# Performance work log

Measured on AMD Instinct MI355X. Metric: run time of the kernel, lower is better.

Reference implementation:

```python
import jax, jax.numpy as jnp
import numpy as np

N = 100000      # nodes
E = 1600000     # edges
B = 64          # graphs in batch
V = 10000       # input_dim (embedding vocab)
EMB = 256       # emb_dim
HID = 64        # hidden_dim
OUT = 32        # output_dim


def setup_inputs() -> dict:
    key = jax.random.key(0)
    ks = jax.random.split(key, 12)
    state = jax.random.randint(ks[0], (B, 2), 0, V, dtype=jnp.int32)
    x = jax.random.randint(ks[1], (N,), 0, V, dtype=jnp.int32)
    edge_index = jax.random.randint(ks[2], (2, E), 0, N, dtype=jnp.int32)
    edge_weight = jnp.ones((E,), jnp.float32)
    # contiguous graph assignment (every graph non-empty)
    batch = jnp.minimum(jnp.arange(N, dtype=jnp.int32) // (N // B), B - 1)

    def lin(k, fin, fout):
        return jax.random.normal(k, (fin, fout), jnp.float32) / np.sqrt(fin).astype(np.float32)

    return {
        "state": state, "x": x, "edge_index": edge_index,
        "edge_weight": edge_weight, "batch": batch,
        "emb_table": jax.random.normal(ks[3], (V, EMB), jnp.float32),
        "W1": lin(ks[4], EMB, HID), "b1": jnp.zeros((HID,), jnp.float32),
        "W2": lin(ks[5], HID, HID), "b2": jnp.zeros((HID,), jnp.float32),
        "Wfc": lin(ks[6], HID, EMB), "bfc": jnp.zeros((EMB,), jnp.float32),
        "Wfc1": lin(ks[7], 3 * EMB, HID), "bfc1": jnp.zeros((HID,), jnp.float32),
        "Wfc2": lin(ks[8], HID, HID), "bfc2": jnp.zeros((HID,), jnp.float32),
        "Wfc3": lin(ks[9], HID, OUT), "bfc3": jnp.zeros((OUT,), jnp.float32),
    }


def gcn_conv(h, src, dst, ew, W, b):
    # PyG GCNConv: linear (no bias) -> sym-normalized aggregation w/ self loops -> + bias
    hw = h @ W                                           # [N, F_out]
    deg = jax.ops.segment_sum(ew, dst, num_segments=N) + 1.0  # +1 for self loop
    dinv = jax.lax.rsqrt(deg)                            # deg >= 1 always
    norm = dinv[src] * ew * dinv[dst]                    # [E]
    agg = jax.ops.segment_sum(norm[:, None] * hw[src], dst, num_segments=N)
    agg = agg + (dinv * dinv)[:, None] * hw              # self-loop contribution
    return agg + b


def reference(state, x, edge_index, edge_weight, batch, emb_table,
              W1, b1, W2, b2, Wfc, bfc, Wfc1, bfc1, Wfc2, bfc2, Wfc3, bfc3):
    src, dst = edge_index[0], edge_index[1]
    h = emb_table[x]                                     # [N, EMB]
    h = jax.nn.relu(gcn_conv(h, src, dst, edge_weight, W1, b1))
    h = gcn_conv(h, src, dst, edge_weight, W2, b2)       # [N, HID]
    # global mean pool over graphs
    counts = jax.ops.segment_sum(jnp.ones((N,), h.dtype), batch, num_segments=B)
    pooled = jax.ops.segment_sum(h, batch, num_segments=B) / jnp.maximum(counts, 1.0)[:, None]
    g = pooled @ Wfc + bfc                               # [B, EMB]
    x1 = emb_table[state[:, 0]]                          # [B, EMB]
    x2 = emb_table[state[:, 1]]                          # [B, EMB]
    z = jnp.concatenate([x1, x2, g], axis=-1)            # [B, 3*EMB]
    z = jax.nn.relu(z @ Wfc1 + bfc1)
    z = jax.nn.relu(z @ Wfc2 + bfc2)
    return z @ Wfc3 + bfc3                               # [B, OUT]
```

## Files before the change

### kernel.cpp

```cpp
#include <hip/hip_runtime.h>

#define NN   100000
#define NE   1600000
#define NB   64
#define NV   10000
#define EMB  256
#define HID  64
#define OUTD 32
#define CAP  64
#define NCH  ((NN + 1023) / 1024)

__device__ __forceinline__ void atomAddF(float* p, float v) {
  __hip_atomic_fetch_add(p, v, __ATOMIC_RELAXED, __HIP_MEMORY_SCOPE_AGENT);
}

__global__ void k_zero(float* p, int n) {
  int i = blockIdx.x * blockDim.x + threadIdx.x;
  if (i < n) p[i] = 0.f;
}

__global__ void k_fill_dir(const int* __restrict__ src, const int* __restrict__ dst,
                           const float* __restrict__ ew,
                           int* cnt, int2* __restrict__ pad, int ne) {
  int e = blockIdx.x * blockDim.x + threadIdx.x;
  if (e < ne) {
    int d = dst[e];
    int pos = atomicAdd(&cnt[d], 1);
    if (pos < CAP) pad[(size_t)d * CAP + pos] = make_int2(src[e], __float_as_int(ew[e]));
  }
}

__global__ void k_cnt_hist(const int* __restrict__ dst, int* cnt, int ne) {
  int e = blockIdx.x * blockDim.x + threadIdx.x;
  if (e < ne) atomicAdd(&cnt[dst[e]], 1);
}

__global__ __launch_bounds__(256) void k_blockred(const int* __restrict__ cnt, int* bsum, int n) {
  __shared__ int sh[256];
  int b = blockIdx.x, t = threadIdx.x;
  int base = b * 1024;
  int s = 0;
  for (int q = 0; q < 4; ++q) {
    int idx = base + q * 256 + t;
    if (idx < n) s += cnt[idx];
  }
  sh[t] = s; __syncthreads();
  for (int off = 128; off > 0; off >>= 1) {
    if (t < off) sh[t] += sh[t + off];
    __syncthreads();
  }
  if (t == 0) bsum[b] = sh[0];
}

__global__ void k_scan_small(int* bsum, int* rowptr, int nch, int n) {
  if (blockIdx.x == 0 && threadIdx.x == 0) {
    int run = 0;
    for (int i = 0; i < nch; ++i) { int t = bsum[i]; bsum[i] = run; run += t; }
    rowptr[n] = run;
  }
}

__global__ __launch_bounds__(256) void k_scan_chunk(const int* __restrict__ cnt,
                                                    const int* __restrict__ bsumx,
                                                    int* __restrict__ rowptr,
                                                    int* __restrict__ cursor, int n) {
  __shared__ int wsumS[4];
  int b = blockIdx.x, t = threadIdx.x, lane = t & 63, w = t >> 6;
  int base = b * 1024 + t * 4;
  int v0 = (base + 0 < n) ? cnt[base + 0] : 0;
  int v1 = (base + 1 < n) ? cnt[base + 1] : 0;
  int v2 = (base + 2 < n) ? cnt[base + 2] : 0;
  int v3 = (base + 3 < n) ? cnt[base + 3] : 0;
  int ts = v0 + v1 + v2 + v3;
  int x = ts;
  for (int d = 1; d < 64; d <<= 1) {
    int y = __shfl_up(x, d);
    if (lane >= d) x += y;
  }
  if (lane == 63) wsumS[w] = x;
  __syncthreads();
  int woff = 0;
  for (int q = 0; q < w; ++q) woff += wsumS[q];
  int excl = bsumx[b] + woff + x - ts;
  if (base + 0 < n) { rowptr[base + 0] = excl;               cursor[base + 0] = excl; }
  if (base + 1 < n) { rowptr[base + 1] = excl + v0;           cursor[base + 1] = excl + v0; }
  if (base + 2 < n) { rowptr[base + 2] = excl + v0 + v1;      cursor[base + 2] = excl + v0 + v1; }
  if (base + 3 < n) { rowptr[base + 3] = excl + v0 + v1 + v2; cursor[base + 3] = excl + v0 + v1 + v2; }
}

__global__ __launch_bounds__(256) void k_fill2(const int* __restrict__ src,
                                               const int* __restrict__ dst,
                                               const float* __restrict__ ew,
                                               int* cursor, int2* __restrict__ pad, int ne) {
  int e = blockIdx.x * blockDim.x + threadIdx.x;
  if (e < ne) {
    int pos = atomicAdd(&cursor[dst[e]], 1);
    pad[pos] = make_int2(src[e], __float_as_int(ew[e]));
  }
}

__global__ __launch_bounds__(256) void k_deg(const int* __restrict__ rowptr,
                                             const int* __restrict__ cnt,
                                             const int2* __restrict__ pad,
                                             float* __restrict__ dinv, int n) {
  int i = blockIdx.x * blockDim.x + threadIdx.x;
  if (i < n) {
    int r0 = rowptr ? rowptr[i] : i * CAP;
    int c  = cnt[i];
    if (!rowptr && c > CAP) c = CAP;
    float s = 1.0f;
    for (int j = r0; j < r0 + c; ++j) s += __int_as_float(pad[j].y);
    dinv[i] = rsqrtf(s);
  }
}

__global__ __launch_bounds__(256) void k_norm(const int* __restrict__ rowptr,
                                              const int* __restrict__ cnt,
                                              const float* __restrict__ dinv,
                                              int2* __restrict__ pad, int n) {
  int i = blockIdx.x * blockDim.x + threadIdx.x;
  if (i < n) {
    int r0 = rowptr ? rowptr[i] : i * CAP;
    int c  = cnt[i];
    if (!rowptr && c > CAP) c = CAP;
    float dd = dinv[i];
    for (int j = r0; j < r0 + c; ++j) {
      int2 e = pad[j];
      pad[j].y = __float_as_int(dinv[e.x] * __int_as_float(e.y) * dd);
    }
  }
}

__global__ __launch_bounds__(256) void k_tab1(const float* __restrict__ emb,
                                              const float* __restrict__ W1,
                                              float* __restrict__ tab, int nv) {
  __shared__ float w1s[EMB * HID];
  int t = threadIdx.x;
  for (int i = t; i < EMB * HID; i += 256) w1s[i] = W1[i];
  __syncthreads();
  int lane = t & 63;
  int wid = __builtin_amdgcn_readfirstlane((blockIdx.x * 256 + t) >> 6);
  int nw = (gridDim.x * 256) >> 6;
  for (int i0 = wid * 4; i0 < nv; i0 += nw * 4) {
    const float* r0 = emb + (size_t)(i0 + 0) * EMB;
    const float* r1 = emb + (size_t)(i0 + 1) * EMB;
    const float* r2 = emb + (size_t)(i0 + 2) * EMB;
    const float* r3 = emb + (size_t)(i0 + 3) * EMB;
    float a0 = 0.f, a1 = 0.f, a2 = 0.f, a3 = 0.f;
#pragma unroll 8
    for (int k = 0; k < EMB; ++k) {
      float wv = w1s[k * HID + lane];
      a0 = fmaf(r0[k], wv, a0);
      a1 = fmaf(r1[k], wv, a1);
      a2 = fmaf(r2[k], wv, a2);
      a3 = fmaf(r3[k], wv, a3);
    }
    tab[(size_t)(i0 + 0) * HID + lane] = a0;
    tab[(size_t)(i0 + 1) * HID + lane] = a1;
    tab[(size_t)(i0 + 2) * HID + lane] = a2;
    tab[(size_t)(i0 + 3) * HID + lane] = a3;
  }
}

__global__ __launch_bounds__(256) void k_gemm2(const float* __restrict__ agg1,
                                               const float* __restrict__ W2,
                                               float* __restrict__ hw2, int n) {
  __shared__ float w2s[HID * HID];
  int t = threadIdx.x;
  for (int i = t; i < HID * HID; i += 256) w2s[i] = W2[i];
  __syncthreads();
  int lane = t & 63;
  int wid = __builtin_amdgcn_readfirstlane((blockIdx.x * 256 + t) >> 6);
  int nw = (gridDim.x * 256) >> 6;
  for (int i0 = wid * 4; i0 < n; i0 += nw * 4) {
    const float* r0 = agg1 + (size_t)(i0 + 0) * HID;
    const float* r1 = agg1 + (size_t)(i0 + 1) * HID;
    const float* r2 = agg1 + (size_t)(i0 + 2) * HID;
    const float* r3 = agg1 + (size_t)(i0 + 3) * HID;
    float a0 = 0.f, a1 = 0.f, a2 = 0.f, a3 = 0.f;
#pragma unroll 8
    for (int k = 0; k < HID; ++k) {
      float wv = w2s[k * HID + lane];
      a0 = fmaf(fmaxf(r0[k], 0.f), wv, a0);
      a1 = fmaf(fmaxf(r1[k], 0.f), wv, a1);
      a2 = fmaf(fmaxf(r2[k], 0.f), wv, a2);
      a3 = fmaf(fmaxf(r3[k], 0.f), wv, a3);
    }
    hw2[(size_t)(i0 + 0) * HID + lane] = a0;
    hw2[(size_t)(i0 + 1) * HID + lane] = a1;
    hw2[(size_t)(i0 + 2) * HID + lane] = a2;
    hw2[(size_t)(i0 + 3) * HID + lane] = a3;
  }
}

__global__ __launch_bounds__(256) void k_agg(const int* __restrict__ rowptr,
                                             const int* __restrict__ cnt,
                                             const int2* __restrict__ pad,
                                             const float* __restrict__ H,
                                             const int* __restrict__ xmap,
                                             const float* __restrict__ dinv,
                                             const float* __restrict__ bias,
                                             float* __restrict__ aggout, int n) {
  int t = threadIdx.x;
  int lane = t & 63;
  int wid = __builtin_amdgcn_readfirstlane((blockIdx.x * 256 + t) >> 6);
  int nw = (gridDim.x * 256) >> 6;
  float bv = bias[lane];
  for (int d = wid; d < n; d += nw) {
    int r0 = __builtin_amdgcn_readfirstlane(rowptr ? rowptr[d] : d * CAP);
    int c  = __builtin_amdgcn_readfirstlane(cnt[d]);
    if (!rowptr && c > CAP) c = CAP;
    int r1 = r0 + c;
    float di = dinv[d];
    int srow = xmap ? xmap[d] : d;
    float acc = di * di * H[(size_t)srow * HID + lane] + bv;
    int j = r0;
    for (; j + 4 <= r1; j += 4) {
      int2 e0 = pad[j + 0];
      int2 e1 = pad[j + 1];
      int2 e2 = pad[j + 2];
      int2 e3 = pad[j + 3];
      int s0 = xmap ? xmap[e0.x] : e0.x;
      int s1 = xmap ? xmap[e1.x] : e1.x;
      int s2 = xmap ? xmap[e2.x] : e2.x;
      int s3 = xmap ? xmap[e3.x] : e3.x;
      acc = fmaf(__int_as_float(e0.y), H[(size_t)s0 * HID + lane], acc);
      acc = fmaf(__int_as_float(e1.y), H[(size_t)s1 * HID + lane], acc);
      acc = fmaf(__int_as_float(e2.y), H[(size_t)s2 * HID + lane], acc);
      acc = fmaf(__int_as_float(e3.y), H[(size_t)s3 * HID + lane], acc);
    }
    for (; j < r1; ++j) {
      int2 e = pad[j];
      int s = xmap ? xmap[e.x] : e.x;
      acc = fmaf(__int_as_float(e.y), H[(size_t)s * HID + lane], acc);
    }
    aggout[(size_t)d * HID + lane] = acc;
  }
}

__global__ __launch_bounds__(256) void k_pool(const float* __restrict__ h,
                                              const int* __restrict__ batch,
                                              float* pooled, float* counts, int n) {
  int t = threadIdx.x;
  int lane = t & 63;
  int gw = (blockIdx.x * 256 + t) >> 6;
  int nw = (gridDim.x * 256) >> 6;
  int per = (n + nw - 1) / nw;
  int s = gw * per;
  int e = min(n, s + per);
  if (s >= e) return;
  int cur = batch[s];
  float acc = 0.f;
  int cnt = 0;
  for (int i = s; i < e; ++i) {
    int b = batch[i];
    if (b != cur) {
      atomAddF(&pooled[cur * HID + lane], acc);
      if (lane == 0) atomAddF(&counts[cur], (float)cnt);
      acc = 0.f; cnt = 0; cur = b;
    }
    acc += h[(size_t)i * HID + lane];
    cnt++;
  }
  atomAddF(&pooled[cur * HID + lane], acc);
  if (lane == 0) atomAddF(&counts[cur], (float)cnt);
}

__global__ __launch_bounds__(256) void k_head(const float* __restrict__ pooled,
                                              const float* __restrict__ counts,
                                              const float* __restrict__ emb,
                                              const int* __restrict__ state,
                                              const float* __restrict__ Wfc,  const float* __restrict__ bfc,
                                              const float* __restrict__ Wfc1, const float* __restrict__ bfc1,
                                              const float* __restrict__ Wfc2, const float* __restrict__ bfc2,
                                              const float* __restrict__ Wfc3, const float* __restrict__ bfc3,
                                              float* __restrict__ out) {
  __shared__ float z[3 * EMB];
  __shared__ float pm[HID];
  __shared__ float h1[HID];
  __shared__ float h2[HID];
  int b = blockIdx.x, t = threadIdx.x;
  if (t < HID) pm[t] = pooled[b * HID + t] / fmaxf(counts[b], 1.0f);
  __syncthreads();
  int s0 = state[2 * b], s1 = state[2 * b + 1];
  z[t]       = emb[(size_t)s0 * EMB + t];
  z[EMB + t] = emb[(size_t)s1 * EMB + t];
  float acc = bfc[t];
  for (int j = 0; j < HID; ++j) acc += pm[j] * Wfc[j * EMB + t];
  z[2 * EMB + t] = acc;
  __syncthreads();
  if (t < HID) {
    float a = bfc1[t];
    for (int k = 0; k < 3 * EMB; ++k) a += z[k] * Wfc1[k * HID + t];
    h1[t] = fmaxf(a, 0.f);
  }
  __syncthreads();
  if (t < HID) {
    float a = bfc2[t];
    for (int k = 0; k < HID; ++k) a += h1[k] * Wfc2[k * HID + t];
    h2[t] = fmaxf(a, 0.f);
  }
  __syncthreads();
  if (t < OUTD) {
    float a = bfc3[t];
    for (int k = 0; k < HID; ++k) a += h2[k] * Wfc3[k * OUTD + t];
    out[b * OUTD + t] = a;
  }
}

extern "C" void kernel_launch(void* const* d_in, const int* in_sizes, int n_in,
                              void* d_out, int out_size, void* d_ws, size_t ws_size,
                              hipStream_t stream) {
  const int*   state = (const int*)d_in[0];
  const int*   x     = (const int*)d_in[1];
  const int*   eidx  = (const int*)d_in[2];
  const int*   src   = eidx;
  const int*   dst   = eidx + NE;
  const float* ew    = (const float*)d_in[3];
  const int*   batch = (const int*)d_in[4];
  const float* emb   = (const float*)d_in[5];
  const float* W1    = (const float*)d_in[6];
  const float* b1    = (const float*)d_in[7];
  const float* W2    = (const float*)d_in[8];
  const float* b2    = (const float*)d_in[9];
  const float* Wfc   = (const float*)d_in[10];
  const float* bfc   = (const float*)d_in[11];
  const float* Wfc1  = (const float*)d_in[12];
  const float* bfc1  = (const float*)d_in[13];
  const float* Wfc2  = (const float*)d_in[14];
  const float* bfc2  = (const float*)d_in[15];
  const float* Wfc3  = (const float*)d_in[16];
  const float* bfc3  = (const float*)d_in[17];
  float* out = (float*)d_out;

  char* p = (char*)d_ws;
  auto alloc = [&](size_t bytes) -> void* {
    void* r = (void*)p;
    p += (bytes + 255) & ~(size_t)255;
    return r;
  };

  const bool direct = ws_size >= 107000000ull;

  float* dinv = (float*)alloc(NN * 4);
  int*   cnt  = (int*)  alloc(NN * 4);
  int*   rowptr = nullptr;
  int*   cursor = nullptr;
  int*   bsum   = nullptr;
  int2*  pad;
  if (direct) {
    pad = (int2*)alloc((size_t)NN * CAP * 8);
  } else {
    rowptr = (int*)alloc((NN + 1) * 4);
    cursor = (int*)alloc(NN * 4);
    bsum   = (int*)alloc(NCH * 4);
    pad    = (int2*)alloc((size_t)NE * 8);
  }
  float* tab1   = (float*)alloc((size_t)NV * HID * 4);
  float* bufA   = (float*)alloc((size_t)NN * HID * 4);
  float* bufB   = (float*)alloc((size_t)NN * HID * 4);
  float* pooled = (float*)alloc(NB * HID * 4);
  float* counts = (float*)alloc(NB * 4);

  dim3 b256(256);
  int gN = (NN + 255) / 256;
  int gE = (NE + 255) / 256;

  k_zero<<<gN, b256, 0, stream>>>((float*)cnt, NN);
  if (direct) {
    k_fill_dir<<<gE, b256, 0, stream>>>(src, dst, ew, cnt, pad, NE);
  } else {
    k_cnt_hist<<<gE, b256, 0, stream>>>(dst, cnt, NE);
    k_blockred<<<NCH, b256, 0, stream>>>(cnt, bsum, NN);
    k_scan_small<<<1, 64, 0, stream>>>(bsum, rowptr, NCH, NN);
    k_scan_chunk<<<NCH, b256, 0, stream>>>(cnt, bsum, rowptr, cursor, NN);
    k_fill2<<<gE, b256, 0, stream>>>(src, dst, ew, cursor, pad, NE);
  }

  k_deg<<<gN, b256, 0, stream>>>(rowptr, cnt, pad, dinv, NN);
  k_norm<<<gN, b256, 0, stream>>>(rowptr, cnt, dinv, pad, NN);

  k_tab1<<<625, b256, 0, stream>>>(emb, W1, tab1, NV);

  k_agg<<<2048, b256, 0, stream>>>(rowptr, cnt, pad, tab1, x, dinv, b1, bufB, NN);

  k_gemm2<<<1024, b256, 0, stream>>>(bufB, W2, bufA, NN);
  k_agg<<<2048, b256, 0, stream>>>(rowptr, cnt, pad, bufA, (const int*)nullptr, dinv, b2, bufB, NN);

  k_zero<<<(NB * HID + NB + 255) / 256, b256, 0, stream>>>(pooled, NB * HID + NB);
  k_pool<<<128, b256, 0, stream>>>(bufB, batch, pooled, counts, NN);

  k_head<<<NB, b256, 0, stream>>>(pooled, counts, emb, state,
                                  Wfc, bfc, Wfc1, bfc1, Wfc2, bfc2, Wfc3, bfc3, out);
}
```

Baseline: 568.9 us.

## Two-level bucket fill of padded adjacency and fold normalization into aggregation

The direct adjacency build now first scatters edges into coarse buckets of 64 destination nodes, packing the local destination into the high bits of the source index. A second per-bucket pass then fills the per-node padded lists, so the writes land in a more local region. The separate edge-normalization pass is removed, and the aggregation kernel computes dinv[src]*w*dinv[dst] on the fly. This saves one read-write sweep over the edge list, at the cost of extra dinv gathers in both aggregation passes. It also carries risks: bucket capacity overflow silently drops edges, the packing assumes source indices fit in 17 bits, and the bucket storage reuses bufA and bufB.

```diff
diff --git a/kernel.cpp b/kernel.cpp
--- a/kernel.cpp
+++ b/kernel.cpp
@@ -8,6 +8,9 @@
 #define HID  64
 #define OUTD 32
 #define CAP  64
+#define BSH  6
+#define NBKT ((NN + 63) >> 6)
+#define BCAP 1536
 #define NCH  ((NN + 1023) / 1024)
 
 __device__ __forceinline__ void atomAddF(float* p, float v) {
@@ -19,14 +22,33 @@
   if (i < n) p[i] = 0.f;
 }
 
-__global__ void k_fill_dir(const int* __restrict__ src, const int* __restrict__ dst,
-                           const float* __restrict__ ew,
-                           int* cnt, int2* __restrict__ pad, int ne) {
+__global__ __launch_bounds__(256) void k_bucket(const int* __restrict__ src,
+                                                const int* __restrict__ dst,
+                                                const float* __restrict__ ew,
+                                                int* bktcur, int2* __restrict__ bkt, int ne) {
   int e = blockIdx.x * blockDim.x + threadIdx.x;
   if (e < ne) {
     int d = dst[e];
+    int b = d >> BSH;
+    int pos = atomicAdd(&bktcur[b], 1);
+    if (pos < BCAP)
+      bkt[(size_t)b * BCAP + pos] = make_int2(src[e] | ((d & 63) << 17), __float_as_int(ew[e]));
+  }
+}
+
+__global__ __launch_bounds__(256) void k_fill_bkt(const int* __restrict__ bktcur,
+                                                  const int2* __restrict__ bkt,
+                                                  int* cnt, int2* __restrict__ pad) {
+  int b = blockIdx.x;
+  int m = bktcur[b];
+  if (m > BCAP) m = BCAP;
+  int based = b << BSH;
+  for (int i = threadIdx.x; i < m; i += 256) {
+    int2 v = bkt[(size_t)b * BCAP + i];
+    int s = v.x & 0x1FFFF;
+    int d = based + (v.x >> 17);
     int pos = atomicAdd(&cnt[d], 1);
-    if (pos < CAP) pad[(size_t)d * CAP + pos] = make_int2(src[e], __float_as_int(ew[e]));
+    if (pos < CAP) pad[(size_t)d * CAP + pos] = make_int2(s, v.y);
   }
 }
 
@@ -111,23 +133,6 @@
     float s = 1.0f;
     for (int j = r0; j < r0 + c; ++j) s += __int_as_float(pad[j].y);
     dinv[i] = rsqrtf(s);
-  }
-}
-
-__global__ __launch_bounds__(256) void k_norm(const int* __restrict__ rowptr,
-                                              const int* __restrict__ cnt,
-                                              const float* __restrict__ dinv,
-                                              int2* __restrict__ pad, int n) {
-  int i = blockIdx.x * blockDim.x + threadIdx.x;
-  if (i < n) {
-    int r0 = rowptr ? rowptr[i] : i * CAP;
-    int c  = cnt[i];
-    if (!rowptr && c > CAP) c = CAP;
-    float dd = dinv[i];
-    for (int j = r0; j < r0 + c; ++j) {
-      int2 e = pad[j];
-      pad[j].y = __float_as_int(dinv[e.x] * __int_as_float(e.y) * dd);
-    }
   }
 }
 
@@ -220,19 +225,24 @@
       int2 e1 = pad[j + 1];
       int2 e2 = pad[j + 2];
       int2 e3 = pad[j + 3];
+      float n0 = dinv[e0.x] * __int_as_float(e0.y) * di;
+      float n1 = dinv[e1.x] * __int_as_float(e1.y) * di;
+      float n2 = dinv[e2.x] * __int_as_float(e2.y) * di;
+      float n3 = dinv[e3.x] * __int_as_float(e3.y) * di;
       int s0 = xmap ? xmap[e0.x] : e0.x;
       int s1 = xmap ? xmap[e1.x] : e1.x;
       int s2 = xmap ? xmap[e2.x] : e2.x;
       int s3 = xmap ? xmap[e3.x] : e3.x;
-      acc = fmaf(__int_as_float(e0.y), H[(size_t)s0 * HID + lane], acc);
-      acc = fmaf(__int_as_float(e1.y), H[(size_t)s1 * HID + lane], acc);
-      acc = fmaf(__int_as_float(e2.y), H[(size_t)s2 * HID + lane], acc);
-      acc = fmaf(__int_as_float(e3.y), H[(size_t)s3 * HID + lane], acc);
+      acc = fmaf(n0, H[(size_t)s0 * HID + lane], acc);
+      acc = fmaf(n1, H[(size_t)s1 * HID + lane], acc);
+      acc = fmaf(n2, H[(size_t)s2 * HID + lane], acc);
+      acc = fmaf(n3, H[(size_t)s3 * HID + lane], acc);
     }
     for (; j < r1; ++j) {
       int2 e = pad[j];
+      float nn = dinv[e.x] * __int_as_float(e.y) * di;
       int s = xmap ? xmap[e.x] : e.x;
-      acc = fmaf(__int_as_float(e.y), H[(size_t)s * HID + lane], acc);
+      acc = fmaf(nn, H[(size_t)s * HID + lane], acc);
     }
     aggout[(size_t)d * HID + lane] = acc;
   }
@@ -362,13 +372,18 @@
   float* pooled = (float*)alloc(NB * HID * 4);
   float* counts = (float*)alloc(NB * 4);
 
+  int2* bkt    = (int2*)bufA;
+  int*  bktcur = (int*)bufB;
+
   dim3 b256(256);
   int gN = (NN + 255) / 256;
   int gE = (NE + 255) / 256;
 
   k_zero<<<gN, b256, 0, stream>>>((float*)cnt, NN);
   if (direct) {
-    k_fill_dir<<<gE, b256, 0, stream>>>(src, dst, ew, cnt, pad, NE);
+    k_zero<<<(NBKT + 255) / 256, b256, 0, stream>>>((float*)bktcur, NBKT);
+    k_bucket<<<gE, b256, 0, stream>>>(src, dst, ew, bktcur, bkt, NE);
+    k_fill_bkt<<<NBKT, b256, 0, stream>>>(bktcur, bkt, cnt, pad);
   } else {
     k_cnt_hist<<<gE, b256, 0, stream>>>(dst, cnt, NE);
     k_blockred<<<NCH, b256, 0, stream>>>(cnt, bsum, NN);
@@ -378,7 +393,6 @@
   }
 
   k_deg<<<gN, b256, 0, stream>>>(rowptr, cnt, pad, dinv, NN);
-  k_norm<<<gN, b256, 0, stream>>>(rowptr, cnt, dinv, pad, NN);
 
   k_tab1<<<625, b256, 0, stream>>>(emb, W1, tab1, NV);
 
```

New measurement: 754.6 us. 32.6% more time.
